# Kernel tuning notes

Hardware: AMD Instinct MI355X
Metric: run time of the kernel (lower is better)

The kernel has to match this reference:

```python
import jax, jax.numpy as jnp
import numpy as np

ALPHA = 0.2  # LeakyReLU negative slope
NEG_INF = -9e15


def _gat_layer(Wh, adj, a, concat):
    """One GraphAttentionLayer given pre-projected Wh [B,N,F].
    Algebraic split of the concat attention: e[b,i,j] = lrelu(Wh[i]@a1 + Wh[j]@a2),
    identical math to matmul(cat(Wh_i, Wh_j), a)."""
    F_ = Wh.shape[-1]
    f1 = Wh @ a[:F_, 0]   # [B,N]
    f2 = Wh @ a[F_:, 0]   # [B,N]
    e = jax.nn.leaky_relu(f1[:, :, None] + f2[:, None, :], negative_slope=ALPHA)  # [B,N,N]
    e = jnp.where(adj > 0, e, NEG_INF)
    att = jax.nn.softmax(e, axis=-1)            # dropout omitted (eval mode)
    h_prime = jnp.einsum('bij,bjf->bif', att, Wh)
    return jax.nn.elu(h_prime) if concat else h_prime


def setup_inputs() -> dict:
    key = jax.random.key(0)
    ks = jax.random.split(key, 9)
    B, N, Fin, H, nH, Fout = 4, 2048, 512, 128, 4, 256
    x = jax.random.normal(ks[0], (B, N, Fin), dtype=jnp.float32)
    adj = jax.random.randint(ks[1], (B, N, N), 0, 2, dtype=jnp.int32)
    mask = jnp.ones((B, N), dtype=jnp.float32)
    s = 0.05
    W_heads = jax.random.normal(ks[2], (nH, Fin, H), dtype=jnp.float32) * s
    a_heads = jax.random.normal(ks[3], (nH, 2 * H, 1), dtype=jnp.float32) * s
    W_out = jax.random.normal(ks[4], (nH * H, Fout), dtype=jnp.float32) * s
    a_out = jax.random.normal(ks[5], (2 * Fout, 1), dtype=jnp.float32) * s
    W_pool = jax.random.normal(ks[6], (Fout, Fout), dtype=jnp.float32) * s
    b_pool = jax.random.normal(ks[7], (Fout,), dtype=jnp.float32) * s
    return {"x": x, "adj": adj, "mask": mask, "W_heads": W_heads, "a_heads": a_heads,
            "W_out": W_out, "a_out": a_out, "W_pool": W_pool, "b_pool": b_pool}


def reference(x, adj, mask, W_heads, a_heads, W_out, a_out, W_pool, b_pool):
    # multi-head GAT layer, heads concatenated (dropout = identity in eval)
    heads = [_gat_layer(x @ W_heads[h], adj, a_heads[h], concat=True)
             for h in range(W_heads.shape[0])]
    xcat = jnp.concatenate(heads, axis=-1)                 # [B,N,nH*H]
    x_out = _gat_layer(xcat @ W_out, adj, a_out, concat=False)  # [B,N,Fout]
    x_out = x_out * mask[:, :, None]
    pooled = x_out.sum(axis=1) / (mask.sum(axis=1, keepdims=True) + 1e-10)
    graph_embedding = jax.nn.relu(pooled @ W_pool + b_pool)
    return graph_embedding, x_out
```

## Files before the change

kernel.cpp:

```cpp
#include <hip/hip_runtime.h>

typedef unsigned short u16;
typedef __attribute__((ext_vector_type(8))) short s8v;
typedef __attribute__((ext_vector_type(8))) unsigned short us8;
typedef __attribute__((ext_vector_type(4))) float f4v;

#define L2E 1.4426950408889634f

typedef __attribute__((address_space(1))) void gvoid_t;
typedef __attribute__((address_space(3))) void lvoid_t;

__device__ __forceinline__ u16 f2bf(float f) {
  unsigned u = __builtin_bit_cast(unsigned, f);
  return (u16)((u + 0x7FFFu + ((u >> 16) & 1u)) >> 16);
}
__device__ __forceinline__ float bf2f(u16 h) {
  return __builtin_bit_cast(float, ((unsigned)h) << 16);
}
__device__ __forceinline__ f4v mfma16(s8v a, s8v b, f4v c) {
  return __builtin_amdgcn_mfma_f32_16x16x32_bf16(a, b, c, 0, 0, 0);
}
__device__ __forceinline__ float exp2fast(float x) {
#if __has_builtin(__builtin_amdgcn_exp2f)
  return __builtin_amdgcn_exp2f(x);
#else
  return exp2f(x);
#endif
}
__device__ __forceinline__ void stage16(const u16* g, u16* lds_arr, int slot) {
#if __has_builtin(__builtin_amdgcn_global_load_lds)
  __builtin_amdgcn_global_load_lds((gvoid_t*)(g),
      (lvoid_t*)(lds_arr + (size_t)(slot & ~63) * 8), 16, 0, 0);
#else
  *(us8*)(lds_arr + (size_t)slot * 8) = *(const us8*)g;
#endif
}

__global__ __launch_bounds__(256) void prep_x(const float* __restrict__ x,
                                              u16* __restrict__ xb) {
  int i = (blockIdx.x * 256 + threadIdx.x) * 8;
  float4 v0 = *(const float4*)(x + i);
  float4 v1 = *(const float4*)(x + i + 4);
  us8 o;
  o[0] = f2bf(v0.x); o[1] = f2bf(v0.y); o[2] = f2bf(v0.z); o[3] = f2bf(v0.w);
  o[4] = f2bf(v1.x); o[5] = f2bf(v1.y); o[6] = f2bf(v1.z); o[7] = f2bf(v1.w);
  *(us8*)(xb + i) = o;
}

__global__ __launch_bounds__(256) void prep_wall(const float* __restrict__ W,
                                                 u16* __restrict__ Wt) {
  int idx = blockIdx.x * 256 + threadIdx.x;
  int h = idx >> 16, k = (idx >> 7) & 511, f = idx & 127;
  Wt[(size_t)(h * 128 + f) * 512 + k] = f2bf(W[idx]);
}
__global__ __launch_bounds__(256) void prep_wout(const float* __restrict__ W,
                                                 u16* __restrict__ Wt) {
  int idx = blockIdx.x * 256 + threadIdx.x;
  int k = idx >> 8, c = idx & 255;
  Wt[(size_t)c * 512 + k] = f2bf(W[idx]);
}
__global__ __launch_bounds__(256) void prep_adj(const int* __restrict__ adj,
                                                unsigned* __restrict__ adjw) {
  int chunk = blockIdx.x * 4 + (threadIdx.x >> 6);
  int l = threadIdx.x & 63;
  int v = adj[(size_t)chunk * 64 + l];
  unsigned long long m = __ballot(v != 0);
  if (l == 0) {
    ((uint2*)adjw)[chunk] = make_uint2((unsigned)m, (unsigned)(m >> 32));
  }
}

__global__ __launch_bounds__(256) void gemm_bf16(const u16* __restrict__ A,
                                                 const u16* __restrict__ Bt,
                                                 u16* __restrict__ Ct, int CO) {
  const int K = 512, N = 2048;
  int m0 = blockIdx.x * 64;
  int n0 = blockIdx.y * 64;
  int t = threadIdx.x;
  int w = t >> 6, l = t & 63, lr = l & 15, lq = l >> 4;
  int wr = w >> 1, wc = w & 1;
  __shared__ u16 As[2][64 * 32];
  __shared__ u16 Bs[2][64 * 32];
  f4v zero4 = {0.f, 0.f, 0.f, 0.f};
  f4v acc[2][2];
#pragma unroll
  for (int i = 0; i < 2; ++i)
#pragma unroll
    for (int j = 0; j < 2; ++j) acc[i][j] = zero4;

  auto stage = [&](int buf, int kt) {
    int k0 = kt * 32;
    int row = t >> 2, ch = t & 3;
    int q = (ch ^ ((row >> 1) & 3)) * 8;
    stage16(A + (size_t)(m0 + row) * K + k0 + q, As[buf], t);
    stage16(Bt + (size_t)(n0 + row) * K + k0 + q, Bs[buf], t);
  };
  stage(0, 0);
  int swz = (lq ^ ((lr >> 1) & 3)) * 8;
  for (int kt = 0; kt < 16; ++kt) {
    __syncthreads();
    if (kt < 15) stage((kt + 1) & 1, kt + 1);
    const u16* as = As[kt & 1];
    const u16* bs = Bs[kt & 1];
    s8v af[2], bfr[2];
#pragma unroll
    for (int rf = 0; rf < 2; ++rf)
      af[rf] = *(const s8v*)&as[(wr * 32 + rf * 16 + lr) * 32 + swz];
#pragma unroll
    for (int nf = 0; nf < 2; ++nf)
      bfr[nf] = *(const s8v*)&bs[(wc * 32 + nf * 16 + lr) * 32 + swz];
#pragma unroll
    for (int rf = 0; rf < 2; ++rf)
#pragma unroll
      for (int nf = 0; nf < 2; ++nf)
        acc[rf][nf] = mfma16(af[rf], bfr[nf], acc[rf][nf]);
  }
  int bidx = m0 >> 11;
  int nr0 = m0 & 2047;
#pragma unroll
  for (int rf = 0; rf < 2; ++rf) {
#pragma unroll
    for (int nf = 0; nf < 2; ++nf) {
      int col = n0 + wc * 32 + nf * 16 + lr;
      int nr = nr0 + wr * 32 + rf * 16 + lq * 4;
      f4v a = acc[rf][nf];
      ushort4 v = make_ushort4(f2bf(a[0]), f2bf(a[1]), f2bf(a[2]), f2bf(a[3]));
      *(ushort4*)&Ct[((size_t)bidx * CO + col) * N + nr] = v;
    }
  }
}

__global__ __launch_bounds__(256) void fkern(const u16* __restrict__ Wht,
                                             const float* __restrict__ a,
                                             float* __restrict__ f1L,
                                             float* __restrict__ f2L, int COLS,
                                             int F) {
  const int N = 2048;
  int h = blockIdx.z, b = blockIdx.y;
  int nl = threadIdx.x & 63, fc = threadIdx.x >> 6;
  int n = blockIdx.x * 64 + nl;
  int F4 = F >> 2;
  const u16* colp = Wht + ((size_t)(b * COLS + h * F + fc * F4)) * N + n;
  const float* ah = a + h * 2 * F + fc * F4;
  float a1 = 0.f, a2 = 0.f;
  for (int c = 0; c < F4; ++c) {
    float v = bf2f(colp[(size_t)c * N]);
    a1 = fmaf(v, ah[c], a1);
    a2 = fmaf(v, ah[F + c], a2);
  }
  __shared__ float r1[4][64], r2[4][64];
  r1[fc][nl] = a1;
  r2[fc][nl] = a2;
  __syncthreads();
  if (fc == 0) {
    float s1 = r1[0][nl] + r1[1][nl] + r1[2][nl] + r1[3][nl];
    float s2 = r2[0][nl] + r2[1][nl] + r2[2][nl] + r2[3][nl];
    f1L[(size_t)(h * 4 + b) * N + n] = s1 * L2E;
    f2L[(size_t)(h * 4 + b) * N + n] = s2 * L2E;
  }
}

__global__ __launch_bounds__(256) void fmax_kern(const float* __restrict__ f2L,
                                                 float* __restrict__ f2m) {
  int row = blockIdx.x;
  const float* p = f2L + (size_t)row * 2048;
  int t = threadIdx.x;
  float v = -__builtin_inff();
  for (int k = 0; k < 8; ++k) v = fmaxf(v, p[t + k * 256]);
#pragma unroll
  for (int d = 1; d < 64; d <<= 1) v = fmaxf(v, __shfl_xor(v, d));
  __shared__ float wm[4];
  if ((t & 63) == 0) wm[t >> 6] = v;
  __syncthreads();
  if (t == 0) f2m[row] = fmaxf(fmaxf(wm[0], wm[1]), fmaxf(wm[2], wm[3]));
}

template <int CT, int WR, bool ELU>
__global__ __launch_bounds__(256, 2) void attn_kernel(
    const u16* __restrict__ Wht, const float* __restrict__ f1L,
    const float* __restrict__ f2L, const float* __restrict__ f2max,
    const unsigned* __restrict__ adjw, const float* __restrict__ mask,
    void* __restrict__ outp) {
  const int N = 2048;
  constexpr int WC = 4 / WR;
  constexpr int NF = 8 / WC;
  constexpr int NCH = CT / 128;
  constexpr int ROWS = WR * 16;
  constexpr int NT = 2048 / ROWS;
  constexpr int FHD = (CT == 512) ? 1 : 0;
  int kb = blockIdx.x;
  int x = kb & 7, g = kb >> 3;
  int p = x + 8 * (g / NT);
  int it = g % NT;
  int b = p / NCH, ch = p % NCH;
  int i0 = it * ROWS, col0 = ch * 128;
  int fh = FHD ? ch : 0;
  int t = threadIdx.x;
  int w = t >> 6, l = t & 63, lr = l & 15, lq = l >> 4;
  int wc = w & (WC - 1), wrs = w / WC;

  __shared__ u16 Vs[2][128 * 64];
  __shared__ unsigned adjs[ROWS * 65];
  __shared__ float f2s[2048];

  const float* f1p = f1L + (size_t)(fh * 4 + b) * N + i0;
  const float* f2p = f2L + (size_t)(fh * 4 + b) * N;
  float f2m = f2max[fh * 4 + b];
  float f1v = f1p[wrs * 16 + lr];
  float su = f1v + f2m;
  float M = fmaxf(su, 0.2f * su);
  float c1 = f1v - M;
  float c2 = 0.2f * f1v - M;
  const u16* vbase = Wht + (size_t)(b * CT + col0) * 2048;

  for (int i = t; i < ROWS * 64; i += 256) {
    int row = i >> 6, wd = i & 63;
    adjs[row * 65 + wd] = adjw[(size_t)(b * N + i0 + row) * 64 + wd];
  }
  for (int i = t; i < 2048; i += 256) f2s[i] = f2p[i];

  auto stage = [&](int buf, int kt) {
    int k0 = kt * 64;
#pragma unroll
    for (int j2 = 0; j2 < 4; ++j2) {
      int s = j2 * 256 + t;
      int c = s >> 3, q = s & 7;
      stage16(vbase + (size_t)c * 2048 + k0 + (q ^ (c & 7)) * 8, Vs[buf], s);
    }
  };
  stage(0, 0);

  f4v zero4 = {0.f, 0.f, 0.f, 0.f};
  f4v acc[NF], accs = zero4;
#pragma unroll
  for (int j = 0; j < NF; ++j) acc[j] = zero4;
  s8v ones;
#pragma unroll
  for (int i = 0; i < 8; ++i) ones[i] = (short)0x3F80;

  for (int kt = 0; kt < 32; ++kt) {
    __syncthreads();
    if (kt < 31) stage((kt + 1) & 1, kt + 1);
    const u16* vs = Vs[kt & 1];
#pragma unroll
    for (int kk = 0; kk < 2; ++kk) {
      int jt = kt * 2 + kk;
      s8v vf[NF];
#pragma unroll
      for (int nf = 0; nf < NF; ++nf) {
        int c = wc * 64 + nf * 16 + lr;
        int chn = (kk * 4 + lq) ^ (lr & 7);
        vf[nf] = *(const s8v*)&vs[c * 64 + chn * 8];
      }
      float4 fa = *(const float4*)&f2s[jt * 32 + lq * 8];
      float4 fb = *(const float4*)&f2s[jt * 32 + lq * 8 + 4];
      float f2c[8] = {fa.x, fa.y, fa.z, fa.w, fb.x, fb.y, fb.z, fb.w};
      unsigned aw = adjs[(wrs * 16 + lr) * 65 + jt];
      union { s8v v; unsigned u[4]; } pk;
#pragma unroll
      for (int ep = 0; ep < 4; ++ep) {
        float t1 = c1 + f2c[2 * ep];
        float t2 = fmaf(0.2f, f2c[2 * ep], c2);
        float p0 = exp2fast(fmaxf(t1, t2));
        p0 = ((aw >> (lq * 8 + 2 * ep)) & 1u) ? p0 : 0.f;
        float t3 = c1 + f2c[2 * ep + 1];
        float t4 = fmaf(0.2f, f2c[2 * ep + 1], c2);
        float p1 = exp2fast(fmaxf(t3, t4));
        p1 = ((aw >> (lq * 8 + 2 * ep + 1)) & 1u) ? p1 : 0.f;
        asm("v_cvt_pk_bf16_f32 %0, %1, %2"
            : "=v"(pk.u[ep]) : "v"(p0), "v"(p1));
      }
      s8v pa = pk.v;
      accs = mfma16(pa, ones, accs);
#pragma unroll
      for (int nf = 0; nf < NF; ++nf)
        acc[nf] = mfma16(pa, vf[nf], acc[nf]);
    }
  }
  f4v i4;
#pragma unroll
  for (int r = 0; r < 4; ++r) i4[r] = 1.f / fmaxf(accs[r], 1e-30f);
  int rowb = i0 + wrs * 16 + lq * 4;
#pragma unroll
  for (int nf = 0; nf < NF; ++nf) {
    int col = col0 + wc * 64 + nf * 16 + lr;
#pragma unroll
    for (int r = 0; r < 4; ++r) {
      float v = acc[nf][r] * i4[r];
      size_t ob = (size_t)(b * N + rowb + r) * CT + col;
      if constexpr (ELU) {
        v = v > 0.f ? v : exp2fast(v * L2E) - 1.f;
        ((u16*)outp)[ob] = f2bf(v);
      } else {
        ((float*)outp)[ob] = v * mask[b * N + rowb + r];
      }
    }
  }
}

__global__ __launch_bounds__(256) void pool1(const float* __restrict__ xout,
                                             const float* __restrict__ mask,
                                             float* __restrict__ pool,
                                             float* __restrict__ den) {
  int b = blockIdx.x >> 6, s = blockIdx.x & 63;
  int c = threadIdx.x;
  int n0 = s * 32;
  float acc = 0.f;
  for (int r = 0; r < 32; ++r)
    acc += xout[((size_t)(b * 2048 + n0 + r)) * 256 + c];
  atomicAdd(&pool[b * 256 + c], acc);
  if (c == 0) {
    float ms = 0.f;
    for (int r = 0; r < 32; ++r) ms += mask[b * 2048 + n0 + r];
    atomicAdd(&den[b], ms);
  }
}
__global__ __launch_bounds__(256) void pool2(const float* __restrict__ pool,
                                             const float* __restrict__ den,
                                             const float* __restrict__ Wp,
                                             const float* __restrict__ bp,
                                             float* __restrict__ out) {
  int b = blockIdx.x, f = threadIdx.x;
  __shared__ float pv[256];
  float inv = 1.f / (den[b] + 1e-10f);
  pv[f] = pool[b * 256 + f] * inv;
  __syncthreads();
  float acc = bp[f];
  for (int c = 0; c < 256; ++c) acc = fmaf(pv[c], Wp[c * 256 + f], acc);
  out[b * 256 + f] = fmaxf(acc, 0.f);
}

extern "C" void kernel_launch(void* const* d_in, const int* in_sizes, int n_in,
                              void* d_out, int out_size, void* d_ws,
                              size_t ws_size, hipStream_t stream) {
  (void)in_sizes; (void)n_in; (void)out_size; (void)ws_size;
  const float* x = (const float*)d_in[0];
  const int* adj = (const int*)d_in[1];
  const float* mask = (const float*)d_in[2];
  const float* Whds = (const float*)d_in[3];
  const float* ahds = (const float*)d_in[4];
  const float* Wout = (const float*)d_in[5];
  const float* aout = (const float*)d_in[6];
  const float* Wpool = (const float*)d_in[7];
  const float* bpool = (const float*)d_in[8];
  float* out = (float*)d_out;

  char* ws = (char*)d_ws;
  size_t off = 0;
  auto take = [&](size_t n) {
    char* p = ws + off;
    off += (n + 255) & ~(size_t)255;
    return p;
  };
  u16* xb = (u16*)take(8192ull * 512 * 2);
  u16* Wta = (u16*)take(512ull * 512 * 2);
  u16* Wto = (u16*)take(256ull * 512 * 2);
  unsigned* adjw = (unsigned*)take(4ull * 2048 * 64 * 4);
  u16* Wht = (u16*)take(4ull * 512 * 2048 * 2);
  float* f1a = (float*)take(4ull * 4 * 2048 * 4);
  float* f2a = (float*)take(4ull * 4 * 2048 * 4);
  u16* xcat = (u16*)take(8192ull * 512 * 2);
  u16* Wh2t = (u16*)take(4ull * 256 * 2048 * 2);
  float* f1b = (float*)take(4ull * 2048 * 4);
  float* f2b = (float*)take(4ull * 2048 * 4);
  float* f2ma = (float*)take(16 * 4);
  float* f2mb = (float*)take(4 * 4);
  float* pool = (float*)take(1024 * 4);
  float* den = (float*)take(256);

  prep_x<<<2048, 256, 0, stream>>>(x, xb);
  prep_wall<<<1024, 256, 0, stream>>>(Whds, Wta);
  prep_wout<<<512, 256, 0, stream>>>(Wout, Wto);
  prep_adj<<<65536, 256, 0, stream>>>(adj, adjw);
  gemm_bf16<<<dim3(128, 8), 256, 0, stream>>>(xb, Wta, Wht, 512);
  fkern<<<dim3(32, 4, 4), 256, 0, stream>>>(Wht, ahds, f1a, f2a, 512, 128);
  fmax_kern<<<16, 256, 0, stream>>>(f2a, f2ma);
  attn_kernel<512, 4, true><<<512, 256, 0, stream>>>(Wht, f1a, f2a, f2ma,
                                                     adjw, nullptr, xcat);
  gemm_bf16<<<dim3(128, 4), 256, 0, stream>>>(xcat, Wto, Wh2t, 256);
  fkern<<<dim3(32, 4, 1), 256, 0, stream>>>(Wh2t, aout, f1b, f2b, 256, 256);
  fmax_kern<<<4, 256, 0, stream>>>(f2b, f2mb);
  attn_kernel<256, 2, false><<<512, 256, 0, stream>>>(Wh2t, f1b, f2b, f2mb,
                                                      adjw, mask, out + 1024);
  hipMemsetAsync(pool, 0, 4096 + 256, stream);
  pool1<<<256, 256, 0, stream>>>(out + 1024, mask, pool, den);
  pool2<<<4, 256, 0, stream>>>(pool, den, Wpool, bpool, out);
}
```

Measured before the change: 174.3 us.

## Merge prep kernels, fuse pooling into attention epilogue, pack score math

Three small weight/input conversion kernels are merged into one launch. The column-sum pooling is folded into the second attention kernel's epilogue using shuffles and atomics, so the separate pool1 pass that re-reads x_out is dropped. The mask denominator is now reduced inside pool2. The LeakyReLU score computation uses two-wide float vectors so it can map to packed FP32 ops. Together these cut launch overhead and one global read of the output, at the cost of more atomics and a different summation order.

```diff
diff --git a/kernel.cpp b/kernel.cpp
--- a/kernel.cpp
+++ b/kernel.cpp
@@ -4,6 +4,7 @@
 typedef __attribute__((ext_vector_type(8))) short s8v;
 typedef __attribute__((ext_vector_type(8))) unsigned short us8;
 typedef __attribute__((ext_vector_type(4))) float f4v;
+typedef __attribute__((ext_vector_type(2))) float fp2;
 
 #define L2E 1.4426950408889634f
 
@@ -36,29 +37,32 @@
 #endif
 }
 
-__global__ __launch_bounds__(256) void prep_x(const float* __restrict__ x,
-                                              u16* __restrict__ xb) {
-  int i = (blockIdx.x * 256 + threadIdx.x) * 8;
-  float4 v0 = *(const float4*)(x + i);
-  float4 v1 = *(const float4*)(x + i + 4);
-  us8 o;
-  o[0] = f2bf(v0.x); o[1] = f2bf(v0.y); o[2] = f2bf(v0.z); o[3] = f2bf(v0.w);
-  o[4] = f2bf(v1.x); o[5] = f2bf(v1.y); o[6] = f2bf(v1.z); o[7] = f2bf(v1.w);
-  *(us8*)(xb + i) = o;
-}
-
-__global__ __launch_bounds__(256) void prep_wall(const float* __restrict__ W,
-                                                 u16* __restrict__ Wt) {
-  int idx = blockIdx.x * 256 + threadIdx.x;
-  int h = idx >> 16, k = (idx >> 7) & 511, f = idx & 127;
-  Wt[(size_t)(h * 128 + f) * 512 + k] = f2bf(W[idx]);
-}
-__global__ __launch_bounds__(256) void prep_wout(const float* __restrict__ W,
-                                                 u16* __restrict__ Wt) {
-  int idx = blockIdx.x * 256 + threadIdx.x;
-  int k = idx >> 8, c = idx & 255;
-  Wt[(size_t)c * 512 + k] = f2bf(W[idx]);
-}
+__global__ __launch_bounds__(256) void prep_all(const float* __restrict__ x,
+                                                u16* __restrict__ xb,
+                                                const float* __restrict__ Wh,
+                                                u16* __restrict__ Wta,
+                                                const float* __restrict__ Wo,
+                                                u16* __restrict__ Wto) {
+  int bid = blockIdx.x;
+  if (bid < 2048) {
+    int i = (bid * 256 + threadIdx.x) * 8;
+    float4 v0 = *(const float4*)(x + i);
+    float4 v1 = *(const float4*)(x + i + 4);
+    us8 o;
+    o[0] = f2bf(v0.x); o[1] = f2bf(v0.y); o[2] = f2bf(v0.z); o[3] = f2bf(v0.w);
+    o[4] = f2bf(v1.x); o[5] = f2bf(v1.y); o[6] = f2bf(v1.z); o[7] = f2bf(v1.w);
+    *(us8*)(xb + i) = o;
+  } else if (bid < 3072) {
+    int idx = (bid - 2048) * 256 + threadIdx.x;
+    int h = idx >> 16, k = (idx >> 7) & 511, f = idx & 127;
+    Wta[(size_t)(h * 128 + f) * 512 + k] = f2bf(Wh[idx]);
+  } else {
+    int idx = (bid - 3072) * 256 + threadIdx.x;
+    int k = idx >> 8, c = idx & 255;
+    Wto[(size_t)c * 512 + k] = f2bf(Wo[idx]);
+  }
+}
+
 __global__ __launch_bounds__(256) void prep_adj(const int* __restrict__ adj,
                                                 unsigned* __restrict__ adjw) {
   int chunk = blockIdx.x * 4 + (threadIdx.x >> 6);
@@ -180,7 +184,7 @@
     const u16* __restrict__ Wht, const float* __restrict__ f1L,
     const float* __restrict__ f2L, const float* __restrict__ f2max,
     const unsigned* __restrict__ adjw, const float* __restrict__ mask,
-    void* __restrict__ outp) {
+    void* __restrict__ outp, float* __restrict__ pool) {
   const int N = 2048;
   constexpr int WC = 4 / WR;
   constexpr int NF = 8 / WC;
@@ -211,6 +215,7 @@
   float M = fmaxf(su, 0.2f * su);
   float c1 = f1v - M;
   float c2 = 0.2f * f1v - M;
+  fp2 c1p = {c1, c1}, c2p = {c2, c2}, k2p = {0.2f, 0.2f};
   const u16* vbase = Wht + (size_t)(b * CT + col0) * 2048;
 
   for (int i = t; i < ROWS * 64; i += 256) {
@@ -255,18 +260,17 @@
       float4 fa = *(const float4*)&f2s[jt * 32 + lq * 8];
       float4 fb = *(const float4*)&f2s[jt * 32 + lq * 8 + 4];
       float f2c[8] = {fa.x, fa.y, fa.z, fa.w, fb.x, fb.y, fb.z, fb.w};
-      unsigned aw = adjs[(wrs * 16 + lr) * 65 + jt];
+      unsigned awl = adjs[(wrs * 16 + lr) * 65 + jt] >> (lq * 8);
       union { s8v v; unsigned u[4]; } pk;
 #pragma unroll
       for (int ep = 0; ep < 4; ++ep) {
-        float t1 = c1 + f2c[2 * ep];
-        float t2 = fmaf(0.2f, f2c[2 * ep], c2);
-        float p0 = exp2fast(fmaxf(t1, t2));
-        p0 = ((aw >> (lq * 8 + 2 * ep)) & 1u) ? p0 : 0.f;
-        float t3 = c1 + f2c[2 * ep + 1];
-        float t4 = fmaf(0.2f, f2c[2 * ep + 1], c2);
-        float p1 = exp2fast(fmaxf(t3, t4));
-        p1 = ((aw >> (lq * 8 + 2 * ep + 1)) & 1u) ? p1 : 0.f;
+        fp2 fpair = {f2c[2 * ep], f2c[2 * ep + 1]};
+        fp2 tA = c1p + fpair;
+        fp2 tB = __builtin_elementwise_fma(k2p, fpair, c2p);
+        float p0 = exp2fast(fmaxf(tA[0], tB[0]));
+        p0 = ((awl >> (2 * ep)) & 1u) ? p0 : 0.f;
+        float p1 = exp2fast(fmaxf(tA[1], tB[1]));
+        p1 = ((awl >> (2 * ep + 1)) & 1u) ? p1 : 0.f;
         asm("v_cvt_pk_bf16_f32 %0, %1, %2"
             : "=v"(pk.u[ep]) : "v"(p0), "v"(p1));
       }
@@ -281,48 +285,56 @@
 #pragma unroll
   for (int r = 0; r < 4; ++r) i4[r] = 1.f / fmaxf(accs[r], 1e-30f);
   int rowb = i0 + wrs * 16 + lq * 4;
-#pragma unroll
-  for (int nf = 0; nf < NF; ++nf) {
-    int col = col0 + wc * 64 + nf * 16 + lr;
-#pragma unroll
-    for (int r = 0; r < 4; ++r) {
-      float v = acc[nf][r] * i4[r];
-      size_t ob = (size_t)(b * N + rowb + r) * CT + col;
-      if constexpr (ELU) {
+  if constexpr (ELU) {
+#pragma unroll
+    for (int nf = 0; nf < NF; ++nf) {
+      int col = col0 + wc * 64 + nf * 16 + lr;
+#pragma unroll
+      for (int r = 0; r < 4; ++r) {
+        float v = acc[nf][r] * i4[r];
         v = v > 0.f ? v : exp2fast(v * L2E) - 1.f;
-        ((u16*)outp)[ob] = f2bf(v);
-      } else {
-        ((float*)outp)[ob] = v * mask[b * N + rowb + r];
+        ((u16*)outp)[(size_t)(b * N + rowb + r) * CT + col] = f2bf(v);
       }
     }
-  }
-}
-
-__global__ __launch_bounds__(256) void pool1(const float* __restrict__ xout,
+  } else {
+    float mk[4];
+#pragma unroll
+    for (int r = 0; r < 4; ++r) mk[r] = mask[b * N + rowb + r];
+#pragma unroll
+    for (int nf = 0; nf < NF; ++nf) {
+      int col = col0 + wc * 64 + nf * 16 + lr;
+      float cs = 0.f;
+#pragma unroll
+      for (int r = 0; r < 4; ++r) {
+        float vm = acc[nf][r] * i4[r] * mk[r];
+        ((float*)outp)[(size_t)(b * N + rowb + r) * CT + col] = vm;
+        cs += vm;
+      }
+      cs += __shfl_xor(cs, 16);
+      cs += __shfl_xor(cs, 32);
+      if (l < 16) atomicAdd(&pool[b * 256 + col], cs);
+    }
+  }
+}
+
+__global__ __launch_bounds__(256) void pool2(const float* __restrict__ pool,
                                              const float* __restrict__ mask,
-                                             float* __restrict__ pool,
-                                             float* __restrict__ den) {
-  int b = blockIdx.x >> 6, s = blockIdx.x & 63;
-  int c = threadIdx.x;
-  int n0 = s * 32;
-  float acc = 0.f;
-  for (int r = 0; r < 32; ++r)
-    acc += xout[((size_t)(b * 2048 + n0 + r)) * 256 + c];
-  atomicAdd(&pool[b * 256 + c], acc);
-  if (c == 0) {
-    float ms = 0.f;
-    for (int r = 0; r < 32; ++r) ms += mask[b * 2048 + n0 + r];
-    atomicAdd(&den[b], ms);
-  }
-}
-__global__ __launch_bounds__(256) void pool2(const float* __restrict__ pool,
-                                             const float* __restrict__ den,
                                              const float* __restrict__ Wp,
                                              const float* __restrict__ bp,
                                              float* __restrict__ out) {
   int b = blockIdx.x, f = threadIdx.x;
   __shared__ float pv[256];
-  float inv = 1.f / (den[b] + 1e-10f);
+  __shared__ float ds[256];
+  float m = 0.f;
+#pragma unroll
+  for (int k = 0; k < 8; ++k) m += mask[b * 2048 + f + k * 256];
+  ds[f] = m;
+  __syncthreads();
+  for (int s = 128; s > 0; s >>= 1) {
+    if (f < s) ds[f] += ds[f + s];
+    __syncthreads();
+  }
+  float inv = 1.f / (ds[0] + 1e-10f);
   pv[f] = pool[b * 256 + f] * inv;
   __syncthreads();
   float acc = bp[f];
@@ -366,23 +378,19 @@
   float* f2ma = (float*)take(16 * 4);
   float* f2mb = (float*)take(4 * 4);
   float* pool = (float*)take(1024 * 4);
-  float* den = (float*)take(256);
-
-  prep_x<<<2048, 256, 0, stream>>>(x, xb);
-  prep_wall<<<1024, 256, 0, stream>>>(Whds, Wta);
-  prep_wout<<<512, 256, 0, stream>>>(Wout, Wto);
+
+  prep_all<<<3584, 256, 0, stream>>>(x, xb, Whds, Wta, Wout, Wto);
   prep_adj<<<65536, 256, 0, stream>>>(adj, adjw);
   gemm_bf16<<<dim3(128, 8), 256, 0, stream>>>(xb, Wta, Wht, 512);
   fkern<<<dim3(32, 4, 4), 256, 0, stream>>>(Wht, ahds, f1a, f2a, 512, 128);
   fmax_kern<<<16, 256, 0, stream>>>(f2a, f2ma);
-  attn_kernel<512, 4, true><<<512, 256, 0, stream>>>(Wht, f1a, f2a, f2ma,
-                                                     adjw, nullptr, xcat);
+  attn_kernel<512, 4, true><<<512, 256, 0, stream>>>(
+      Wht, f1a, f2a, f2ma, adjw, nullptr, xcat, nullptr);
   gemm_bf16<<<dim3(128, 4), 256, 0, stream>>>(xcat, Wto, Wh2t, 256);
   fkern<<<dim3(32, 4, 1), 256, 0, stream>>>(Wh2t, aout, f1b, f2b, 256, 256);
   fmax_kern<<<4, 256, 0, stream>>>(f2b, f2mb);
-  attn_kernel<256, 2, false><<<512, 256, 0, stream>>>(Wh2t, f1b, f2b, f2mb,
-                                                      adjw, mask, out + 1024);
-  hipMemsetAsync(pool, 0, 4096 + 256, stream);
-  pool1<<<256, 256, 0, stream>>>(out + 1024, mask, pool, den);
-  pool2<<<4, 256, 0, stream>>>(pool, den, Wpool, bpool, out);
-}
+  hipMemsetAsync(pool, 0, 1024 * 4, stream);
+  attn_kernel<256, 2, false><<<512, 256, 0, stream>>>(
+      Wh2t, f1b, f2b, f2mb, adjw, mask, out + 1024, pool);
+  pool2<<<4, 256, 0, stream>>>(pool, mask, Wpool, bpool, out);
+}
```

Measured after the change: 167.4 us (median of 2 runs). 4.0% less time.
